# Performance work log

Hardware: AMD Instinct MI355X
Metric: run time of the kernel (lower is better)

Reference implementation:

```python
import jax
jax.config.update("jax_enable_x64", True)
import jax.numpy as jnp
import numpy as np

NUM = 1_000_000
DIM = 128
K = 8


def mueller_hash(t):
    # Matches torch int64 semantics: arithmetic shift, XOR, wrapping multiply.
    t = (t >> 16 ^ t) * 73244475
    t = (t >> 16 ^ t) * 73244475
    t = t >> 16 ^ t
    return t


def setup_inputs() -> dict:
    key = jax.random.key(0)
    k1, k2 = jax.random.split(key)
    t = jax.random.randint(k1, (32, 2048), 0, 1_000_000_000, dtype=jnp.int64)
    # vocab = nn.Linear(dim, num) -> weight shape [num, dim]
    W = jax.random.normal(k2, (NUM, DIM), dtype=jnp.float32) * 0.02
    return {"t": t, "W": W}


def reference(t, W):
    # All k hash probes vectorized: idx [B, S, K]
    r = jnp.arange(K, dtype=t.dtype)
    idx = mueller_hash(t[..., None] + r) % NUM  # jnp.mod matches torch % sign-of-divisor semantics
    # Gather [B, S, K, DIM] then average over the K probes (== sum of W[idx]/K).
    out = jnp.take(W, idx, axis=0).mean(axis=-2)
    return out.astype(jnp.float32)
```

## Files before the change

### kernel.cpp

```cpp
#include <hip/hip_runtime.h>
#include <hip/hip_bf16.h>

constexpr int NUM = 1000000;
constexpr int DIM = 128;

__device__ __forceinline__ int bloom_idx(long long t) {
    long long s = t;
    s = (long long)(((unsigned long long)((s >> 16) ^ s)) * 73244475ull);
    s = (long long)(((unsigned long long)((s >> 16) ^ s)) * 73244475ull);
    s = (s >> 16) ^ s;
    long long m = s % (long long)NUM;
    if (m < 0) m += NUM;
    return (int)m;
}

__global__ __launch_bounds__(256) void bloom_embed_kernel(
        const int* __restrict__ t,
        const float* __restrict__ W,
        float* __restrict__ out,
        int n_tokens) {
    const int gtid  = blockIdx.x * blockDim.x + threadIdx.x;
    const int token = gtid >> 6;
    const int lane  = threadIdx.x & 63;
    if (token >= n_tokens) return;

    const long long tv = (long long)t[token];
    const int my_idx = bloom_idx(tv + (long long)(lane & 7));

    float2 acc = make_float2(0.f, 0.f);
#pragma unroll
    for (int k = 0; k < 8; ++k) {
        const int idx = __shfl(my_idx, k);
        const float2* row = (const float2*)(W + (size_t)idx * DIM);
        const float2 v = row[lane];
        acc.x += v.x;
        acc.y += v.y;
    }
    acc.x *= 0.125f;
    acc.y *= 0.125f;

    ((float2*)(out + (size_t)token * DIM))[lane] = acc;
}

extern "C" void kernel_launch(void* const* d_in, const int* in_sizes, int n_in,
                              void* d_out, int out_size, void* d_ws, size_t ws_size,
                              hipStream_t stream) {
    const int*   t = (const int*)d_in[0];
    const float* W = (const float*)d_in[1];
    float*     out = (float*)d_out;

    const int n_tokens = in_sizes[0];
    const int waves_per_block = 256 / 64;
    const int blocks = (n_tokens + waves_per_block - 1) / waves_per_block;

    bloom_embed_kernel<<<blocks, 256, 0, stream>>>(t, W, out, n_tokens);
}
```

Baseline: 602.3 us.

## Process two tokens per wave with float4 row loads and cross-half shuffle reduction

Each 64-lane wave now handles two tokens instead of one. Each half-wave fetches a full 512-byte embedding row with 16-byte float4 loads, so every load instruction now moves more bytes. Partial sums for the even and odd probes of each token are combined with an xor-32 shuffle before a single float4 store. This cuts the number of waves and load instructions per gathered row, at the cost of extra shuffles and some register pressure.

After: 603.3 us. About the same (+0.2%).

```diff
diff --git a/kernel.cpp b/kernel.cpp
--- a/kernel.cpp
+++ b/kernel.cpp
@@ -1,5 +1,4 @@
 #include <hip/hip_runtime.h>
-#include <hip/hip_bf16.h>
 
 constexpr int NUM = 1000000;
 constexpr int DIM = 128;
@@ -19,27 +18,50 @@
         const float* __restrict__ W,
         float* __restrict__ out,
         int n_tokens) {
-    const int gtid  = blockIdx.x * blockDim.x + threadIdx.x;
-    const int token = gtid >> 6;
-    const int lane  = threadIdx.x & 63;
-    if (token >= n_tokens) return;
+    const int gtid   = blockIdx.x * blockDim.x + threadIdx.x;
+    const int wave   = gtid >> 6;
+    const int lane   = threadIdx.x & 63;
+    const int token0 = wave * 2;
+    if (token0 >= n_tokens) return;
+    const bool have2 = (token0 + 1) < n_tokens;
 
-    const long long tv = (long long)t[token];
+    const int toff = (lane >> 3) & 1;
+    const long long tv = (long long)t[have2 ? (token0 + toff) : token0];
     const int my_idx = bloom_idx(tv + (long long)(lane & 7));
 
-    float2 acc = make_float2(0.f, 0.f);
+    const int half = lane >> 5;
+    const int col  = lane & 31;
+
+    float4 acc0 = make_float4(0.f, 0.f, 0.f, 0.f);
+    float4 acc1 = make_float4(0.f, 0.f, 0.f, 0.f);
 #pragma unroll
-    for (int k = 0; k < 8; ++k) {
-        const int idx = __shfl(my_idx, k);
-        const float2* row = (const float2*)(W + (size_t)idx * DIM);
-        const float2 v = row[lane];
-        acc.x += v.x;
-        acc.y += v.y;
+    for (int j = 0; j < 8; ++j) {
+        const int idx = __shfl(my_idx, 2 * j + half);
+        const float4 v = *(const float4*)(W + (size_t)idx * DIM + col * 4);
+        if (j < 4) {
+            acc0.x += v.x; acc0.y += v.y; acc0.z += v.z; acc0.w += v.w;
+        } else {
+            acc1.x += v.x; acc1.y += v.y; acc1.z += v.z; acc1.w += v.w;
+        }
     }
-    acc.x *= 0.125f;
-    acc.y *= 0.125f;
 
-    ((float2*)(out + (size_t)token * DIM))[lane] = acc;
+    const float4 p = half ? acc1 : acc0;
+    const float4 q = half ? acc0 : acc1;
+    float4 r;
+    r.x = __shfl_xor(q.x, 32);
+    r.y = __shfl_xor(q.y, 32);
+    r.z = __shfl_xor(q.z, 32);
+    r.w = __shfl_xor(q.w, 32);
+
+    float4 val;
+    val.x = (p.x + r.x) * 0.125f;
+    val.y = (p.y + r.y) * 0.125f;
+    val.z = (p.z + r.z) * 0.125f;
+    val.w = (p.w + r.w) * 0.125f;
+
+    if (have2 || half == 0) {
+        ((float4*)(out + (size_t)token0 * DIM))[lane] = val;
+    }
 }
 
 extern "C" void kernel_launch(void* const* d_in, const int* in_sizes, int n_in,
@@ -50,8 +72,9 @@
     float*     out = (float*)d_out;
 
     const int n_tokens = in_sizes[0];
+    const int n_waves  = (n_tokens + 1) / 2;
     const int waves_per_block = 256 / 64;
-    const int blocks = (n_tokens + waves_per_block - 1) / waves_per_block;
+    const int blocks = (n_waves + waves_per_block - 1) / waves_per_block;
 
     bloom_embed_kernel<<<blocks, 256, 0, stream>>>(t, W, out, n_tokens);
 }
```

## Process four tokens per wave with 16-byte nontemporal loads and half-wave reduction

Applied to the files above, without the earlier changes.

Each wave now handles four tokens instead of one. The two half-waves each fetch alternating hash rows with 16-byte vector loads, and the halves are combined with an xor-32 shuffle. Loads and stores use nontemporal hints, and the launch grid is reduced to a quarter. This aims to put more bytes in flight per instruction and amortize the hash computation. The cost is extra cross-lane shuffles and a scalar tail path for leftover tokens.

Result: no change. 592.6 us (-1.6%).

```diff
diff --git a/kernel.cpp b/kernel.cpp
--- a/kernel.cpp
+++ b/kernel.cpp
@@ -1,8 +1,10 @@
 #include <hip/hip_runtime.h>
-#include <hip/hip_bf16.h>
 
 constexpr int NUM = 1000000;
 constexpr int DIM = 128;
+
+typedef float f4 __attribute__((ext_vector_type(4)));
+typedef float f2 __attribute__((ext_vector_type(2)));
 
 __device__ __forceinline__ int bloom_idx(long long t) {
     long long s = t;
@@ -14,32 +16,77 @@
     return (int)m;
 }
 
+__device__ __forceinline__ f4 xor32(f4 a) {
+    f4 r;
+    r.x = __shfl_xor(a.x, 32);
+    r.y = __shfl_xor(a.y, 32);
+    r.z = __shfl_xor(a.z, 32);
+    r.w = __shfl_xor(a.w, 32);
+    return r;
+}
+
 __global__ __launch_bounds__(256) void bloom_embed_kernel(
         const int* __restrict__ t,
         const float* __restrict__ W,
         float* __restrict__ out,
         int n_tokens) {
-    const int gtid  = blockIdx.x * blockDim.x + threadIdx.x;
-    const int token = gtid >> 6;
-    const int lane  = threadIdx.x & 63;
-    if (token >= n_tokens) return;
+    const int gtid   = blockIdx.x * blockDim.x + threadIdx.x;
+    const int wave   = gtid >> 6;
+    const int lane   = threadIdx.x & 63;
+    const int token0 = wave * 4;
+    if (token0 >= n_tokens) return;
 
-    const long long tv = (long long)t[token];
-    const int my_idx = bloom_idx(tv + (long long)(lane & 7));
+    if (token0 + 3 < n_tokens) {
+        const int slot = lane & 31;
+        const int toff = slot >> 3;
+        const long long tv = (long long)t[token0 + toff];
+        const int my_idx = bloom_idx(tv + (long long)(slot & 7));
 
-    float2 acc = make_float2(0.f, 0.f);
+        const int half = lane >> 5;
+        const int col  = lane & 31;
+
+        f4 acc0 = {0.f, 0.f, 0.f, 0.f};
+        f4 acc1 = {0.f, 0.f, 0.f, 0.f};
+        f4 acc2 = {0.f, 0.f, 0.f, 0.f};
+        f4 acc3 = {0.f, 0.f, 0.f, 0.f};
 #pragma unroll
-    for (int k = 0; k < 8; ++k) {
-        const int idx = __shfl(my_idx, k);
-        const float2* row = (const float2*)(W + (size_t)idx * DIM);
-        const float2 v = row[lane];
-        acc.x += v.x;
-        acc.y += v.y;
+        for (int j = 0; j < 16; ++j) {
+            const int idx = __shfl(my_idx, 2 * j + half);
+            const f4 v = __builtin_nontemporal_load(
+                (const f4*)(W + (size_t)idx * DIM) + col);
+            switch (j >> 2) {
+                case 0: acc0 += v; break;
+                case 1: acc1 += v; break;
+                case 2: acc2 += v; break;
+                default: acc3 += v; break;
+            }
+        }
+
+        const f4 v0 = (acc0 + xor32(acc0)) * 0.125f;
+        const f4 v1 = (acc1 + xor32(acc1)) * 0.125f;
+        const f4 v2 = (acc2 + xor32(acc2)) * 0.125f;
+        const f4 v3 = (acc3 + xor32(acc3)) * 0.125f;
+
+        const f4 sA = half ? v1 : v0;
+        const f4 sB = half ? v3 : v2;
+        f4* dst = (f4*)(out + (size_t)token0 * DIM);
+        __builtin_nontemporal_store(sA, dst + lane);
+        __builtin_nontemporal_store(sB, dst + 64 + lane);
+    } else {
+        for (int token = token0; token < n_tokens; ++token) {
+            const long long tv = (long long)t[token];
+            const int my_idx = bloom_idx(tv + (long long)(lane & 7));
+            f2 acc = {0.f, 0.f};
+#pragma unroll
+            for (int k = 0; k < 8; ++k) {
+                const int idx = __shfl(my_idx, k);
+                const f2 v = *((const f2*)(W + (size_t)idx * DIM) + lane);
+                acc += v;
+            }
+            acc *= 0.125f;
+            *((f2*)(out + (size_t)token * DIM) + lane) = acc;
+        }
     }
-    acc.x *= 0.125f;
-    acc.y *= 0.125f;
-
-    ((float2*)(out + (size_t)token * DIM))[lane] = acc;
 }
 
 extern "C" void kernel_launch(void* const* d_in, const int* in_sizes, int n_in,
@@ -50,8 +97,9 @@
     float*     out = (float*)d_out;
 
     const int n_tokens = in_sizes[0];
+    const int n_waves  = (n_tokens + 3) / 4;
     const int waves_per_block = 256 / 64;
-    const int blocks = (n_tokens + waves_per_block - 1) / waves_per_block;
+    const int blocks = (n_waves + waves_per_block - 1) / waves_per_block;
 
     bloom_embed_kernel<<<blocks, 256, 0, stream>>>(t, W, out, n_tokens);
 }
```
